# Performance work log

Measured on AMD Instinct MI355X. Metric: run time of the kernel, lower is better.

Reference implementation:

```python
import jax, jax.numpy as jnp
import numpy as np

B, S, D, H, L, DFF, NI, AD = 8, 512, 512, 8, 4, 2048, 20000, 128
DK = D // H


def _make_pe(max_len, d):
    pos = np.arange(max_len, dtype=np.float32)[:, None]
    div = np.exp(np.arange(0, d, 2, dtype=np.float32) * (-np.log(10000.0) / d))
    pe = np.zeros((max_len, d), dtype=np.float32)
    pe[:, 0::2] = np.sin(pos * div)
    pe[:, 1::2] = np.cos(pos * div)
    return jnp.asarray(pe)


def setup_inputs() -> dict:
    key = jax.random.key(0)
    ks = iter(jax.random.split(key, 64))
    def nrm(shape):
        return jax.random.normal(next(ks), shape, jnp.float32) * 0.02
    inp = {
        'item_ids': jax.random.randint(next(ks), (B, S), 0, NI),
        'audio_features': jax.random.normal(next(ks), (B, S, AD), jnp.float32),
        'is_organic': jax.random.bernoulli(next(ks), 0.5, (B, S)).astype(jnp.float32),
        'padding_mask': jnp.ones((B, 1, 1, S), jnp.float32),
        'emb_table': nrm((NI + 1, D)),
        'pe': _make_pe(S, D),
        'Wa1': nrm((AD, D)), 'ba1': jnp.zeros((D,)),
        'Wa2': nrm((D, D)), 'ba2': jnp.zeros((D,)),
        'Wf': nrm((2 * D, D)), 'bf': jnp.zeros((D,)),
        'Wq': nrm((L, D, D)), 'bq': jnp.zeros((L, D)),
        'Wk': nrm((L, D, D)), 'bk': jnp.zeros((L, D)),
        'Wv': nrm((L, D, D)), 'bv': jnp.zeros((L, D)),
        'Wo': nrm((L, D, D)), 'bo': jnp.zeros((L, D)),
        'worg': nrm((L, H)), 'borg': jnp.zeros((L, H)),
        'ln1s': jnp.ones((L, D)), 'ln1b': jnp.zeros((L, D)),
        'ln2s': jnp.ones((L, D)), 'ln2b': jnp.zeros((L, D)),
        'Wff1': nrm((L, D, DFF)), 'bff1': jnp.zeros((L, DFF)),
        'Wff2': nrm((L, DFF, D)), 'bff2': jnp.zeros((L, D)),
        'lnOs': jnp.ones((D,)), 'lnOb': jnp.zeros((D,)),
        'Wg': nrm((D + 1, D)), 'bg': jnp.zeros((D,)),
        'Wout': nrm((D, NI)), 'bout': jnp.zeros((NI,)),
    }
    return inp


def _ln(x, s, b, eps=1e-5):
    m = jnp.mean(x, -1, keepdims=True)
    v = jnp.mean((x - m) ** 2, -1, keepdims=True)
    return (x - m) * jax.lax.rsqrt(v + eps) * s + b


def reference(item_ids, audio_features, is_organic, padding_mask, emb_table, pe,
              Wa1, ba1, Wa2, ba2, Wf, bf, Wq, bq, Wk, bk, Wv, bv, Wo, bo,
              worg, borg, ln1s, ln1b, ln2s, ln2b, Wff1, bff1, Wff2, bff2,
              lnOs, lnOb, Wg, bg, Wout, bout):
    b_, s_ = item_ids.shape
    scale = 1.0 / np.sqrt(DK).astype(np.float32)
    tbl = emb_table.at[0].set(0.0)  # padding_idx=0
    item_emb = tbl[item_ids]                                    # (B,S,D)
    audio_emb = jax.nn.relu(audio_features @ Wa1 + ba1) @ Wa2 + ba2
    x = jax.nn.relu(jnp.concatenate([item_emb, audio_emb], -1) @ Wf + bf)
    x = x + pe[:s_]
    for l in range(L):
        q = (x @ Wq[l] + bq[l]).reshape(b_, s_, H, DK).transpose(0, 2, 1, 3)
        k = (x @ Wk[l] + bk[l]).reshape(b_, s_, H, DK).transpose(0, 2, 1, 3)
        v = (x @ Wv[l] + bv[l]).reshape(b_, s_, H, DK).transpose(0, 2, 1, 3)
        scores = jnp.einsum('bhqd,bhkd->bhqk', q, k) * scale    # (B,H,S,S)
        org = is_organic[:, :, None] * worg[l] + borg[l]        # (B,S,H)
        scores = scores + org.transpose(0, 2, 1)[..., None]     # per-query bias
        scores = jnp.where(padding_mask == 0, -1e9, scores)
        attn = jax.nn.softmax(scores, -1)
        ctx = jnp.einsum('bhqk,bhkd->bhqd', attn, v)
        ctx = ctx.transpose(0, 2, 1, 3).reshape(b_, s_, D)
        x = _ln(x + ctx @ Wo[l] + bo[l], ln1s[l], ln1b[l])
        ff = jax.nn.relu(x @ Wff1[l] + bff1[l]) @ Wff2[l] + bff2[l]
        x = _ln(x + ff, ln2s[l], ln2b[l])
    x = _ln(x, lnOs, lnOb)
    gate = jax.nn.sigmoid(jnp.concatenate([x, is_organic[..., None]], -1) @ Wg + bg)
    logits = (x * gate) @ Wout + bout                           # (B,S,NI)
    return logits
```

## Files before the change

kernel.cpp:

```cpp
#include <hip/hip_runtime.h>
#include <hip/hip_bf16.h>

typedef float f32x4 __attribute__((ext_vector_type(4)));
typedef __bf16 bf16x8 __attribute__((ext_vector_type(8)));

#define DEV __device__ __forceinline__

constexpr int B_ = 8, S_ = 512, D_ = 512, H_ = 8, L_ = 4, DFF_ = 2048, NI_ = 20000, AD_ = 128, DK_ = 64;
constexpr int N_ = B_ * S_;
constexpr int NOUT_PAD = 20096;

DEV void gload_lds16(const void* g, void* l) {
  __builtin_amdgcn_global_load_lds((const __attribute__((address_space(1))) unsigned int*)g,
                                   (__attribute__((address_space(3))) unsigned int*)l, 16, 0, 0);
}

DEV int xcd_swizzle(int bid, int nwg) {
  int q = nwg >> 3, r = nwg & 7;
  int x = bid & 7, idx = bid >> 3;
  int base = (x < r) ? x * (q + 1) : r * (q + 1) + (x - r) * q;
  return base + idx;
}

template<int BM, int BN, int OUT_BF16, int ACT, int NT>
__global__ __launch_bounds__(BM * 2)
void gemm_bt(const __hip_bfloat16* __restrict__ A, int lda, long aS1, long aS2,
             const __hip_bfloat16* __restrict__ Bm, int ldb, long bS1, long bS2,
             void* __restrict__ Cv, int ldc, long cS1, long cS2,
             const float* __restrict__ bias, long biasS2,
             int K, int Ncols, int bdiv)
{
  constexpr int BK = 32;
  constexpr int NW = BM / 32;
  constexpr int WTN = BN / 2, NJ = WTN / 16;
  __shared__ __align__(16) unsigned short smA[2][BM * BK];
  __shared__ __align__(16) unsigned short smB[2][BN * BK];

  const int z = blockIdx.z;
  const long za = (long)(z / bdiv) * aS1 + (long)(z % bdiv) * aS2;
  const long zb = (long)(z / bdiv) * bS1 + (long)(z % bdiv) * bS2;
  const long zc = (long)(z / bdiv) * cS1 + (long)(z % bdiv) * cS2;
  const __hip_bfloat16* Ab = A + za;
  const __hip_bfloat16* Bp = Bm + zb;
  const float* bp = bias ? bias + (long)(z % bdiv) * biasS2 : nullptr;

  const int nwg = gridDim.x * gridDim.y;
  const int bid = blockIdx.y * gridDim.x + blockIdx.x;
  const int wgid = xcd_swizzle(bid, nwg);
  const int m0 = (wgid % gridDim.x) * BM, n0 = (wgid / gridDim.x) * BN;

  const int tid = threadIdx.x, wv = tid >> 6, lane = tid & 63;
  const int l15 = lane & 15, l4 = lane >> 4;
  const int wm = (wv >> 1) * 64, wn = (wv & 1) * WTN;

  auto stage = [&](int buf, int k0) {
#pragma unroll
    for (int it = 0; it < BM / 16 / NW; ++it) {
      int c = (it * NW + wv) * 64 + lane;
      int row = c >> 2, cc = c & 3;
      gload_lds16((const void*)(Ab + (size_t)(m0 + row) * lda + k0 + cc * 8),
                  (void*)&smA[buf][(size_t)(it * NW + wv) * 512]);
    }
#pragma unroll
    for (int it = 0; it < BN / 16 / NW; ++it) {
      int c = (it * NW + wv) * 64 + lane;
      int row = c >> 2, cc = c & 3;
      gload_lds16((const void*)(Bp + (size_t)(n0 + row) * ldb + k0 + cc * 8),
                  (void*)&smB[buf][(size_t)(it * NW + wv) * 512]);
    }
  };

  f32x4 acc[4][NJ];
#pragma unroll
  for (int i = 0; i < 4; ++i)
#pragma unroll
    for (int j = 0; j < NJ; ++j) acc[i][j] = f32x4{0.f, 0.f, 0.f, 0.f};

  const int nk = K / BK;
  stage(0, 0);
  __syncthreads();

  int cur = 0;
  for (int t = 0; t < nk; ++t) {
    if (t + 1 < nk) stage(cur ^ 1, (t + 1) * BK);

    bf16x8 af[4], bfr[NJ];
#pragma unroll
    for (int i = 0; i < 4; ++i)
      af[i] = *reinterpret_cast<const bf16x8*>(&smA[cur][(wm + i * 16 + l15) * BK + l4 * 8]);
#pragma unroll
    for (int j = 0; j < NJ; ++j)
      bfr[j] = *reinterpret_cast<const bf16x8*>(&smB[cur][(wn + j * 16 + l15) * BK + l4 * 8]);
    __builtin_amdgcn_s_setprio(1);
#pragma unroll
    for (int i = 0; i < 4; ++i)
#pragma unroll
      for (int j = 0; j < NJ; ++j)
        acc[i][j] = __builtin_amdgcn_mfma_f32_16x16x32_bf16(af[i], bfr[j], acc[i][j], 0, 0, 0);
    __builtin_amdgcn_s_setprio(0);
    __syncthreads();
    cur ^= 1;
  }

#pragma unroll
  for (int i = 0; i < 4; ++i) {
#pragma unroll
    for (int j = 0; j < NJ; ++j) {
#pragma unroll
      for (int r = 0; r < 4; ++r) {
        int row = m0 + wm + i * 16 + l4 * 4 + r;
        int col = n0 + wn + j * 16 + l15;
        if (col < Ncols) {
          float v = acc[i][j][r];
          if (bp) v += bp[col];
          if (ACT == 1) v = v > 0.f ? v : 0.f;
          if constexpr (OUT_BF16) {
            ((__hip_bfloat16*)Cv)[zc + (size_t)row * ldc + col] = __float2bfloat16(v);
          } else {
            float* dst = &((float*)Cv)[zc + (size_t)row * ldc + col];
            if constexpr (NT) __builtin_nontemporal_store(v, dst);
            else *dst = v;
          }
        }
      }
    }
  }
}

__global__ __launch_bounds__(256)
void k_flash(const __hip_bfloat16* __restrict__ q, const __hip_bfloat16* __restrict__ k,
             const __hip_bfloat16* __restrict__ vt, const float* __restrict__ mask,
             __hip_bfloat16* __restrict__ ctx)
{
  __shared__ __align__(16) unsigned short Ql[64 * 64];
  __shared__ __align__(16) unsigned short Kl[2][64 * 64];
  __shared__ __align__(16) unsigned short Vl[2][64 * 64];
  __shared__ __align__(16) unsigned short Pl[4][16 * 64];

  const int qt = blockIdx.x, bh = blockIdx.y;
  const int b = bh >> 3, h = bh & 7;
  const int tid = threadIdx.x, wv = tid >> 6, lane = tid & 63;
  const int l15 = lane & 15, l4 = lane >> 4;
  const int q0 = qt * 64;

  const __hip_bfloat16* Qg = q + ((size_t)(b * 512 + q0) * 512) + h * 64;
  const __hip_bfloat16* Kg = k + ((size_t)(b * 512) * 512) + h * 64;
  const __hip_bfloat16* Vg = vt + ((size_t)bh * 64) * 512;
  const float* mk = mask + b * 512;

  auto stageQ = [&]() {
#pragma unroll
    for (int it = 0; it < 2; ++it) {
      int idx = it * 256 + wv * 64 + lane;
      int row = idx >> 3, c = idx & 7;
      gload_lds16((const void*)(Qg + (size_t)row * 512 + (c ^ (row & 7)) * 8),
                  (void*)&Ql[(it * 256 + wv * 64) * 8]);
    }
  };
  auto stageKV = [&](int buf, int kv0) {
#pragma unroll
    for (int it = 0; it < 2; ++it) {
      int idx = it * 256 + wv * 64 + lane;
      int row = idx >> 3, c = idx & 7;
      gload_lds16((const void*)(Kg + (size_t)(kv0 + row) * 512 + (c ^ (row & 7)) * 8),
                  (void*)&Kl[buf][(it * 256 + wv * 64) * 8]);
    }
#pragma unroll
    for (int it = 0; it < 2; ++it) {
      int idx = it * 256 + wv * 64 + lane;
      int row = idx >> 3, c = idx & 7;
      gload_lds16((const void*)(Vg + (size_t)row * 512 + kv0 + (c ^ (row & 7)) * 8),
                  (void*)&Vl[buf][(it * 256 + wv * 64) * 8]);
    }
  };

  stageQ();
  stageKV(0, 0);
  __syncthreads();

  bf16x8 aq[2];
#pragma unroll
  for (int kk = 0; kk < 2; ++kk) {
    int row = wv * 16 + l15;
    aq[kk] = *reinterpret_cast<const bf16x8*>(
        &Ql[row * 64 + (((kk * 4 + l4) ^ (row & 7)) * 8)]);
  }

  f32x4 accO[4];
  float mrun[4], lrun[4];
#pragma unroll
  for (int j = 0; j < 4; ++j) accO[j] = f32x4{0.f, 0.f, 0.f, 0.f};
#pragma unroll
  for (int r = 0; r < 4; ++r) { mrun[r] = -3e38f; lrun[r] = 0.f; }

  int cur = 0;
  for (int t = 0; t < 8; ++t) {
    if (t + 1 < 8) stageKV(cur ^ 1, (t + 1) * 64);
    const int kv0 = t * 64;

    f32x4 s[4];
#pragma unroll
    for (int j = 0; j < 4; ++j) s[j] = f32x4{0.f, 0.f, 0.f, 0.f};
#pragma unroll
    for (int kk = 0; kk < 2; ++kk) {
#pragma unroll
      for (int j = 0; j < 4; ++j) {
        int row = j * 16 + l15;
        bf16x8 bk = *reinterpret_cast<const bf16x8*>(
            &Kl[cur][row * 64 + (((kk * 4 + l4) ^ (row & 7)) * 8)]);
        s[j] = __builtin_amdgcn_mfma_f32_16x16x32_bf16(aq[kk], bk, s[j], 0, 0, 0);
      }
    }

#pragma unroll
    for (int j = 0; j < 4; ++j) {
      float mval = mk[kv0 + j * 16 + l15];
#pragma unroll
      for (int r = 0; r < 4; ++r)
        s[j][r] = (mval == 0.f) ? -1e30f : s[j][r];
    }

    float alpha[4];
#pragma unroll
    for (int r = 0; r < 4; ++r) {
      float v = fmaxf(fmaxf(s[0][r], s[1][r]), fmaxf(s[2][r], s[3][r]));
      v = fmaxf(v, __shfl_xor(v, 1));
      v = fmaxf(v, __shfl_xor(v, 2));
      v = fmaxf(v, __shfl_xor(v, 4));
      v = fmaxf(v, __shfl_xor(v, 8));
      float mn = fmaxf(mrun[r], v);
      alpha[r] = __expf(mrun[r] - mn);
      mrun[r] = mn;
    }
    float rs[4] = {0.f, 0.f, 0.f, 0.f};
#pragma unroll
    for (int j = 0; j < 4; ++j)
#pragma unroll
      for (int r = 0; r < 4; ++r) {
        float p = __expf(s[j][r] - mrun[r]);
        s[j][r] = p;
        rs[r] += p;
      }
#pragma unroll
    for (int r = 0; r < 4; ++r) {
      float v = rs[r];
      v += __shfl_xor(v, 1); v += __shfl_xor(v, 2);
      v += __shfl_xor(v, 4); v += __shfl_xor(v, 8);
      lrun[r] = lrun[r] * alpha[r] + v;
#pragma unroll
      for (int j = 0; j < 4; ++j) accO[j][r] *= alpha[r];
    }

#pragma unroll
    for (int j = 0; j < 4; ++j)
#pragma unroll
      for (int r = 0; r < 4; ++r) {
        int qrow = l4 * 4 + r, key = j * 16 + l15;
        __hip_bfloat16 hb = __float2bfloat16(s[j][r]);
        Pl[wv][qrow * 64 + (((key >> 3) ^ (qrow & 7)) * 8) + (key & 7)] =
            *reinterpret_cast<unsigned short*>(&hb);
      }

#pragma unroll
    for (int kc = 0; kc < 2; ++kc) {
      bf16x8 ap = *reinterpret_cast<const bf16x8*>(
          &Pl[wv][l15 * 64 + (((kc * 4 + l4) ^ (l15 & 7)) * 8)]);
#pragma unroll
      for (int j = 0; j < 4; ++j) {
        int row = j * 16 + l15;
        bf16x8 bv2 = *reinterpret_cast<const bf16x8*>(
            &Vl[cur][row * 64 + (((kc * 4 + l4) ^ (row & 7)) * 8)]);
        accO[j] = __builtin_amdgcn_mfma_f32_16x16x32_bf16(ap, bv2, accO[j], 0, 0, 0);
      }
    }
    __syncthreads();
    cur ^= 1;
  }

#pragma unroll
  for (int r = 0; r < 4; ++r) {
    float inv = lrun[r] > 0.f ? 1.f / lrun[r] : 0.f;
#pragma unroll
    for (int j = 0; j < 4; ++j) {
      int row = q0 + wv * 16 + l4 * 4 + r;
      int col = h * 64 + j * 16 + l15;
      ctx[(size_t)(b * 512 + row) * 512 + col] = __float2bfloat16(accO[j][r] * inv);
    }
  }
}

__global__ void k_transpose(const float* __restrict__ in, __hip_bfloat16* __restrict__ out,
                            int K, int N, long inBatch, long outBatch, float scale)
{
  __shared__ float tile[32][33];
  int z = blockIdx.z;
  const float* ip = in + (long)z * inBatch;
  __hip_bfloat16* op = out + (long)z * outBatch;
  int n0 = blockIdx.x * 32, k0 = blockIdx.y * 32;
  int tx = threadIdx.x, ty = threadIdx.y;
#pragma unroll
  for (int r = 0; r < 4; ++r) {
    int k = k0 + ty + r * 8, n = n0 + tx;
    if (k < K && n < N) tile[ty + r * 8][tx] = ip[(size_t)k * N + n];
  }
  __syncthreads();
#pragma unroll
  for (int r = 0; r < 4; ++r) {
    int n = n0 + ty + r * 8, k = k0 + tx;
    if (n < N && k < K) op[(size_t)n * K + k] = __float2bfloat16(tile[tx][ty + r * 8] * scale);
  }
}

__global__ void k_cvt(const float* __restrict__ in, __hip_bfloat16* __restrict__ out) {
  int i = blockIdx.x * 256 + threadIdx.x;
  out[i] = __float2bfloat16(in[i]);
}

__global__ void k_packbias(const float* __restrict__ bq, const float* __restrict__ bk,
                           const float* __restrict__ bv, float* __restrict__ out) {
  int i = blockIdx.x * 256 + threadIdx.x;
  int d = i & 511, t = (i >> 9) % 3, l = i / (3 * 512);
  const float* src = (t == 0) ? bq : (t == 1) ? bk : bv;
  out[i] = src[l * 512 + d] * (t == 0 ? 0.125f : 1.f);
}

__global__ void k_gather(const int* __restrict__ ids, const float* __restrict__ tbl,
                         __hip_bfloat16* __restrict__ cat) {
  int n = blockIdx.x, t = threadIdx.x;
  int id = ids[n];
  const float* src = tbl + (size_t)id * 512;
  size_t dst = (size_t)n * 1024;
  float a0 = (id == 0) ? 0.f : src[t];
  float a1 = (id == 0) ? 0.f : src[t + 256];
  cat[dst + t] = __float2bfloat16(a0);
  cat[dst + t + 256] = __float2bfloat16(a1);
}

__global__ void k_peadd(float* __restrict__ xf, __hip_bfloat16* __restrict__ xb,
                        const float* __restrict__ pe) {
  int i = blockIdx.x * 256 + threadIdx.x;
  float v = xf[i] + pe[i & (S_ * D_ - 1)];
  xf[i] = v;
  xb[i] = __float2bfloat16(v);
}

__global__ void k_vtrans(const __hip_bfloat16* __restrict__ v, __hip_bfloat16* __restrict__ vt) {
  int i = blockIdx.x * 256 + threadIdx.x;
  int s = i & 511, d = (i >> 9) & 63, h = (i >> 15) & 7, b = i >> 18;
  vt[i] = v[(size_t)((b << 9) + s) * 512 + (h << 6) + d];
}

__global__ void k_ln(const float* __restrict__ x, const float* __restrict__ y,
                     const float* __restrict__ gam, const float* __restrict__ bet,
                     float* __restrict__ xout, __hip_bfloat16* __restrict__ xb) {
  int row = blockIdx.x, t = threadIdx.x;
  size_t base = (size_t)row * 512;
  float v0 = x[base + t], v1 = x[base + t + 256];
  if (y) { v0 += y[base + t]; v1 += y[base + t + 256]; }
  __shared__ float sm[4];
  float s = v0 + v1;
  for (int o = 32; o; o >>= 1) s += __shfl_xor(s, o);
  if ((t & 63) == 0) sm[t >> 6] = s;
  __syncthreads();
  float mean = (sm[0] + sm[1] + sm[2] + sm[3]) * (1.f / 512.f);
  __syncthreads();
  float d0 = v0 - mean, d1 = v1 - mean;
  float qq = d0 * d0 + d1 * d1;
  for (int o = 32; o; o >>= 1) qq += __shfl_xor(qq, o);
  if ((t & 63) == 0) sm[t >> 6] = qq;
  __syncthreads();
  float var = (sm[0] + sm[1] + sm[2] + sm[3]) * (1.f / 512.f);
  float rs = rsqrtf(var + 1e-5f);
  float o0 = d0 * rs * gam[t] + bet[t];
  float o1 = d1 * rs * gam[t + 256] + bet[t + 256];
  xout[base + t] = o0;
  xout[base + t + 256] = o1;
  xb[base + t] = __float2bfloat16(o0);
  xb[base + t + 256] = __float2bfloat16(o1);
}

__global__ void k_gate(const float* __restrict__ xn, const float* __restrict__ g,
                       const float* __restrict__ org, const float* __restrict__ wgl,
                       __hip_bfloat16* __restrict__ xg) {
  int i = blockIdx.x * 256 + threadIdx.x;
  float zz = g[i] + org[i >> 9] * wgl[i & 511];
  float sg = 1.f / (1.f + expf(-zz));
  xg[i] = __float2bfloat16(xn[i] * sg);
}

extern "C" void kernel_launch(void* const* d_in, const int* in_sizes, int n_in,
                              void* d_out, int out_size, void* d_ws, size_t ws_size,
                              hipStream_t stream) {
  typedef __hip_bfloat16 bf;
  const int*   item_ids = (const int*)  d_in[0];
  const float* audio    = (const float*)d_in[1];
  const float* organic  = (const float*)d_in[2];
  const float* mask     = (const float*)d_in[3];
  const float* emb      = (const float*)d_in[4];
  const float* pe       = (const float*)d_in[5];
  const float* Wa1 = (const float*)d_in[6],  *ba1 = (const float*)d_in[7];
  const float* Wa2 = (const float*)d_in[8],  *ba2 = (const float*)d_in[9];
  const float* Wf  = (const float*)d_in[10], *bfb = (const float*)d_in[11];
  const float* Wq  = (const float*)d_in[12], *bq  = (const float*)d_in[13];
  const float* Wk  = (const float*)d_in[14], *bk  = (const float*)d_in[15];
  const float* Wv  = (const float*)d_in[16], *bv  = (const float*)d_in[17];
  const float* Wo  = (const float*)d_in[18], *bo  = (const float*)d_in[19];
  const float* ln1s = (const float*)d_in[22], *ln1b = (const float*)d_in[23];
  const float* ln2s = (const float*)d_in[24], *ln2b = (const float*)d_in[25];
  const float* Wff1 = (const float*)d_in[26], *bff1 = (const float*)d_in[27];
  const float* Wff2 = (const float*)d_in[28], *bff2 = (const float*)d_in[29];
  const float* lnOs = (const float*)d_in[30], *lnOb = (const float*)d_in[31];
  const float* Wg   = (const float*)d_in[32], *bg   = (const float*)d_in[33];
  const float* Wout = (const float*)d_in[34], *bout = (const float*)d_in[35];
  float* out = (float*)d_out;

  char* ws = (char*)d_ws;
  size_t off = 0;
  auto alloc = [&](size_t bytes) -> char* {
    char* p = ws + off;
    off = (off + bytes + 255) & ~(size_t)255;
    return p;
  };
  bf* Wa1T = (bf*)alloc((size_t)512 * 128 * 2);
  bf* Wa2T = (bf*)alloc((size_t)512 * 512 * 2);
  bf* WfT  = (bf*)alloc((size_t)512 * 1024 * 2);
  bf* WqkvT = (bf*)alloc((size_t)L_ * 3 * D_ * D_ * 2);
  bf* WoT  = (bf*)alloc((size_t)L_ * D_ * D_ * 2);
  bf* Wff1T = (bf*)alloc((size_t)L_ * DFF_ * D_ * 2);
  bf* Wff2T = (bf*)alloc((size_t)L_ * D_ * DFF_ * 2);
  bf* WgT   = (bf*)alloc((size_t)512 * 512 * 2);
  bf* WoutT = (bf*)alloc((size_t)NOUT_PAD * 512 * 2);
  float* bqkv = (float*)alloc((size_t)L_ * 3 * 512 * 4);
  bf* ab    = (bf*)alloc((size_t)N_ * AD_ * 2);
  bf* cat   = (bf*)alloc((size_t)N_ * 1024 * 2);
  bf* ah    = (bf*)alloc((size_t)N_ * 512 * 2);
  float* xf = (float*)alloc((size_t)N_ * 512 * 4);
  bf* xb    = (bf*)alloc((size_t)N_ * 512 * 2);
  bf* qkv   = (bf*)alloc((size_t)3 * N_ * 512 * 2);
  bf* vt    = (bf*)alloc((size_t)B_ * H_ * DK_ * S_ * 2);
  bf* ctxb  = (bf*)alloc((size_t)N_ * 512 * 2);
  float* ybuf = (float*)alloc((size_t)N_ * 512 * 4);
  bf* ff1b  = (bf*)alloc((size_t)N_ * DFF_ * 2);
  bf* xg    = (bf*)alloc((size_t)N_ * 512 * 2);
  if (off > ws_size) return;

  bf* qb = qkv;
  bf* kb = qkv + (size_t)N_ * 512;
  bf* vb = qkv + (size_t)2 * N_ * 512;

  dim3 tb(32, 8);
  k_transpose<<<dim3(16, 4, 1),  tb, 0, stream>>>(Wa1, Wa1T, 128, 512, 0, 0, 1.f);
  k_transpose<<<dim3(16, 16, 1), tb, 0, stream>>>(Wa2, Wa2T, 512, 512, 0, 0, 1.f);
  k_transpose<<<dim3(16, 32, 1), tb, 0, stream>>>(Wf, WfT, 1024, 512, 0, 0, 1.f);
  k_transpose<<<dim3(16, 16, L_), tb, 0, stream>>>(Wq, WqkvT, 512, 512,
      (long)D_ * D_, (long)3 * D_ * D_, 0.125f);
  k_transpose<<<dim3(16, 16, L_), tb, 0, stream>>>(Wk, WqkvT + (size_t)D_ * D_, 512, 512,
      (long)D_ * D_, (long)3 * D_ * D_, 1.f);
  k_transpose<<<dim3(16, 16, L_), tb, 0, stream>>>(Wv, WqkvT + (size_t)2 * D_ * D_, 512, 512,
      (long)D_ * D_, (long)3 * D_ * D_, 1.f);
  k_transpose<<<dim3(16, 16, L_), tb, 0, stream>>>(Wo, WoT, 512, 512, (long)D_ * D_, (long)D_ * D_, 1.f);
  k_transpose<<<dim3(64, 16, L_), tb, 0, stream>>>(Wff1, Wff1T, 512, 2048, (long)D_ * DFF_, (long)D_ * DFF_, 1.f);
  k_transpose<<<dim3(16, 64, L_), tb, 0, stream>>>(Wff2, Wff2T, 2048, 512, (long)DFF_ * D_, (long)DFF_ * D_, 1.f);
  k_transpose<<<dim3(16, 16, 1), tb, 0, stream>>>(Wg, WgT, 512, 512, 0, 0, 1.f);
  k_transpose<<<dim3(625, 16, 1), tb, 0, stream>>>(Wout, WoutT, 512, 20000, 0, 0, 1.f);
  k_packbias<<<(L_ * 3 * 512) / 256, 256, 0, stream>>>(bq, bk, bv, bqkv);

  k_cvt<<<(N_ * AD_) / 256, 256, 0, stream>>>(audio, ab);
  k_gather<<<N_, 256, 0, stream>>>(item_ids, emb, cat);
  gemm_bt<128, 64, 1, 1, 0><<<dim3(32, 8, 1), 256, 0, stream>>>(ab, 128, 0, 0, Wa1T, 128, 0, 0,
      (void*)ah, 512, 0, 0, ba1, 0, 128, 512, 1);
  gemm_bt<128, 64, 1, 0, 0><<<dim3(32, 8, 1), 256, 0, stream>>>(ah, 512, 0, 0, Wa2T, 512, 0, 0,
      (void*)(cat + 512), 1024, 0, 0, ba2, 0, 512, 512, 1);
  gemm_bt<128, 64, 0, 1, 0><<<dim3(32, 8, 1), 256, 0, stream>>>(cat, 1024, 0, 0, WfT, 1024, 0, 0,
      (void*)xf, 512, 0, 0, bfb, 0, 1024, 512, 1);
  k_peadd<<<(N_ * D_) / 256, 256, 0, stream>>>(xf, xb, pe);

  for (int l = 0; l < L_; ++l) {
    gemm_bt<128, 64, 1, 0, 0><<<dim3(32, 8, 3), 256, 0, stream>>>(xb, 512, 0, 0,
        WqkvT + (size_t)l * 3 * D_ * D_, 512, 0, (long)D_ * D_,
        (void*)qkv, 512, 0, (long)N_ * D_,
        bqkv + (size_t)l * 3 * 512, 512, 512, 512, 3);
    k_vtrans<<<(B_ * H_ * DK_ * S_) / 256, 256, 0, stream>>>(vb, vt);
    k_flash<<<dim3(8, B_ * H_), 256, 0, stream>>>(qb, kb, vt, mask, ctxb);
    gemm_bt<128, 64, 0, 0, 0><<<dim3(32, 8, 1), 256, 0, stream>>>(ctxb, 512, 0, 0,
        WoT + (size_t)l * D_ * D_, 512, 0, 0, (void*)ybuf, 512, 0, 0, bo + l * D_, 0, 512, 512, 1);
    k_ln<<<N_, 256, 0, stream>>>(xf, ybuf, ln1s + l * D_, ln1b + l * D_, xf, xb);
    gemm_bt<256, 128, 1, 1, 0><<<dim3(16, 16, 1), 512, 0, stream>>>(xb, 512, 0, 0,
        Wff1T + (size_t)l * DFF_ * D_, 512, 0, 0, (void*)ff1b, 2048, 0, 0, bff1 + l * DFF_, 0, 512, 2048, 1);
    gemm_bt<128, 64, 0, 0, 0><<<dim3(32, 8, 1), 256, 0, stream>>>(ff1b, 2048, 0, 0,
        Wff2T + (size_t)l * D_ * DFF_, 2048, 0, 0, (void*)ybuf, 512, 0, 0, bff2 + l * D_, 0, 2048, 512, 1);
    k_ln<<<N_, 256, 0, stream>>>(xf, ybuf, ln2s + l * D_, ln2b + l * D_, xf, xb);
  }

  k_ln<<<N_, 256, 0, stream>>>(xf, nullptr, lnOs, lnOb, xf, xb);
  gemm_bt<128, 64, 0, 0, 0><<<dim3(32, 8, 1), 256, 0, stream>>>(xb, 512, 0, 0, WgT, 512, 0, 0,
      (void*)ybuf, 512, 0, 0, bg, 0, 512, 512, 1);
  k_gate<<<(N_ * D_) / 256, 256, 0, stream>>>(xf, ybuf, organic, Wg + (size_t)512 * 512, xg);
  gemm_bt<256, 128, 0, 0, 1><<<dim3(16, 157, 1), 512, 0, stream>>>(xg, 512, 0, 0, WoutT, 512, 0, 0,
      (void*)out, 20000, 0, 0, bout, 0, 512, 20000, 1);
}
```

Baseline: 890.9 us.

## Replace double-buffered GEMM with 4-stage vmcnt-pipelined kernel and smaller tiles

The GEMM kernel moves from a double-buffered loop with two __syncthreads per k-step to a 4-buffer ring that keeps three k-tiles of global-to-LDS loads in flight. It waits with explicit s_waitcnt vmcnt counts and uses a single barrier per step. The FF1 and output-projection GEMMs also move from 256x128 tiles on 512 threads to 128x128 tiles on 256 threads, which doubles the grid. The aim is to hide global load latency and improve occupancy, at the cost of more LDS per block and hand-coded wait counts that must match the number of loads issued.

```diff
diff --git a/kernel.cpp b/kernel.cpp
--- a/kernel.cpp
+++ b/kernel.cpp
@@ -13,6 +13,14 @@
 DEV void gload_lds16(const void* g, void* l) {
   __builtin_amdgcn_global_load_lds((const __attribute__((address_space(1))) unsigned int*)g,
                                    (__attribute__((address_space(3))) unsigned int*)l, 16, 0, 0);
+}
+
+template<int N> DEV void waitv() {
+  if constexpr (N == 0)      asm volatile("s_waitcnt vmcnt(0)" ::: "memory");
+  else if constexpr (N == 3) asm volatile("s_waitcnt vmcnt(3)" ::: "memory");
+  else if constexpr (N == 4) asm volatile("s_waitcnt vmcnt(4)" ::: "memory");
+  else if constexpr (N == 6) asm volatile("s_waitcnt vmcnt(6)" ::: "memory");
+  else if constexpr (N == 8) asm volatile("s_waitcnt vmcnt(8)" ::: "memory");
 }
 
 DEV int xcd_swizzle(int bid, int nwg) {
@@ -23,18 +31,18 @@
 }
 
 template<int BM, int BN, int OUT_BF16, int ACT, int NT>
-__global__ __launch_bounds__(BM * 2)
-void gemm_bt(const __hip_bfloat16* __restrict__ A, int lda, long aS1, long aS2,
-             const __hip_bfloat16* __restrict__ Bm, int ldb, long bS1, long bS2,
-             void* __restrict__ Cv, int ldc, long cS1, long cS2,
-             const float* __restrict__ bias, long biasS2,
-             int K, int Ncols, int bdiv)
+__global__ __launch_bounds__(256)
+void gemm_p(const __hip_bfloat16* __restrict__ A, int lda, long aS1, long aS2,
+            const __hip_bfloat16* __restrict__ Bm, int ldb, long bS1, long bS2,
+            void* __restrict__ Cv, int ldc, long cS1, long cS2,
+            const float* __restrict__ bias, long biasS2,
+            int K, int Ncols, int bdiv)
 {
-  constexpr int BK = 32;
-  constexpr int NW = BM / 32;
-  constexpr int WTN = BN / 2, NJ = WTN / 16;
-  __shared__ __align__(16) unsigned short smA[2][BM * BK];
-  __shared__ __align__(16) unsigned short smB[2][BN * BK];
+  constexpr int BK = 32, NB = 4;
+  constexpr int MI = BM / 32, NJ = BN / 32;
+  constexpr int LT = BM / 64 + BN / 64;
+  __shared__ __align__(16) unsigned short smA[NB][BM * BK];
+  __shared__ __align__(16) unsigned short smB[NB][BN * BK];
 
   const int z = blockIdx.z;
   const long za = (long)(z / bdiv) * aS1 + (long)(z % bdiv) * aS2;
@@ -51,59 +59,64 @@
 
   const int tid = threadIdx.x, wv = tid >> 6, lane = tid & 63;
   const int l15 = lane & 15, l4 = lane >> 4;
-  const int wm = (wv >> 1) * 64, wn = (wv & 1) * WTN;
+  const int wm = (wv >> 1) * (BM / 2), wn = (wv & 1) * (BN / 2);
 
   auto stage = [&](int buf, int k0) {
 #pragma unroll
-    for (int it = 0; it < BM / 16 / NW; ++it) {
-      int c = (it * NW + wv) * 64 + lane;
+    for (int it = 0; it < BM / 64; ++it) {
+      int c = it * 256 + tid;
       int row = c >> 2, cc = c & 3;
       gload_lds16((const void*)(Ab + (size_t)(m0 + row) * lda + k0 + cc * 8),
-                  (void*)&smA[buf][(size_t)(it * NW + wv) * 512]);
-    }
-#pragma unroll
-    for (int it = 0; it < BN / 16 / NW; ++it) {
-      int c = (it * NW + wv) * 64 + lane;
+                  (void*)&smA[buf][(size_t)(it * 256 + wv * 64) * 8]);
+    }
+#pragma unroll
+    for (int it = 0; it < BN / 64; ++it) {
+      int c = it * 256 + tid;
       int row = c >> 2, cc = c & 3;
       gload_lds16((const void*)(Bp + (size_t)(n0 + row) * ldb + k0 + cc * 8),
-                  (void*)&smB[buf][(size_t)(it * NW + wv) * 512]);
+                  (void*)&smB[buf][(size_t)(it * 256 + wv * 64) * 8]);
     }
   };
 
-  f32x4 acc[4][NJ];
-#pragma unroll
-  for (int i = 0; i < 4; ++i)
+  f32x4 acc[MI][NJ];
+#pragma unroll
+  for (int i = 0; i < MI; ++i)
 #pragma unroll
     for (int j = 0; j < NJ; ++j) acc[i][j] = f32x4{0.f, 0.f, 0.f, 0.f};
 
   const int nk = K / BK;
   stage(0, 0);
-  __syncthreads();
-
-  int cur = 0;
+  stage(1, BK);
+  stage(2, 2 * BK);
+
   for (int t = 0; t < nk; ++t) {
-    if (t + 1 < nk) stage(cur ^ 1, (t + 1) * BK);
-
-    bf16x8 af[4], bfr[NJ];
-#pragma unroll
-    for (int i = 0; i < 4; ++i)
+    if (t + 2 < nk)      waitv<2 * LT>();
+    else if (t + 1 < nk) waitv<LT>();
+    else                 waitv<0>();
+    __builtin_amdgcn_s_barrier();
+    __builtin_amdgcn_sched_barrier(0);
+
+    if (t + 3 < nk) stage((t + 3) & 3, (t + 3) * BK);
+
+    const int cur = t & 3;
+    bf16x8 af[MI], bfr[NJ];
+#pragma unroll
+    for (int i = 0; i < MI; ++i)
       af[i] = *reinterpret_cast<const bf16x8*>(&smA[cur][(wm + i * 16 + l15) * BK + l4 * 8]);
 #pragma unroll
     for (int j = 0; j < NJ; ++j)
       bfr[j] = *reinterpret_cast<const bf16x8*>(&smB[cur][(wn + j * 16 + l15) * BK + l4 * 8]);
     __builtin_amdgcn_s_setprio(1);
 #pragma unroll
-    for (int i = 0; i < 4; ++i)
+    for (int i = 0; i < MI; ++i)
 #pragma unroll
       for (int j = 0; j < NJ; ++j)
         acc[i][j] = __builtin_amdgcn_mfma_f32_16x16x32_bf16(af[i], bfr[j], acc[i][j], 0, 0, 0);
     __builtin_amdgcn_s_setprio(0);
-    __syncthreads();
-    cur ^= 1;
-  }
-
-#pragma unroll
-  for (int i = 0; i < 4; ++i) {
+  }
+
+#pragma unroll
+  for (int i = 0; i < MI; ++i) {
 #pragma unroll
     for (int j = 0; j < NJ; ++j) {
 #pragma unroll
@@ -467,35 +480,35 @@
 
   k_cvt<<<(N_ * AD_) / 256, 256, 0, stream>>>(audio, ab);
   k_gather<<<N_, 256, 0, stream>>>(item_ids, emb, cat);
-  gemm_bt<128, 64, 1, 1, 0><<<dim3(32, 8, 1), 256, 0, stream>>>(ab, 128, 0, 0, Wa1T, 128, 0, 0,
+  gemm_p<128, 64, 1, 1, 0><<<dim3(32, 8, 1), 256, 0, stream>>>(ab, 128, 0, 0, Wa1T, 128, 0, 0,
       (void*)ah, 512, 0, 0, ba1, 0, 128, 512, 1);
-  gemm_bt<128, 64, 1, 0, 0><<<dim3(32, 8, 1), 256, 0, stream>>>(ah, 512, 0, 0, Wa2T, 512, 0, 0,
+  gemm_p<128, 64, 1, 0, 0><<<dim3(32, 8, 1), 256, 0, stream>>>(ah, 512, 0, 0, Wa2T, 512, 0, 0,
       (void*)(cat + 512), 1024, 0, 0, ba2, 0, 512, 512, 1);
-  gemm_bt<128, 64, 0, 1, 0><<<dim3(32, 8, 1), 256, 0, stream>>>(cat, 1024, 0, 0, WfT, 1024, 0, 0,
+  gemm_p<128, 64, 0, 1, 0><<<dim3(32, 8, 1), 256, 0, stream>>>(cat, 1024, 0, 0, WfT, 1024, 0, 0,
       (void*)xf, 512, 0, 0, bfb, 0, 1024, 512, 1);
   k_peadd<<<(N_ * D_) / 256, 256, 0, stream>>>(xf, xb, pe);
 
   for (int l = 0; l < L_; ++l) {
-    gemm_bt<128, 64, 1, 0, 0><<<dim3(32, 8, 3), 256, 0, stream>>>(xb, 512, 0, 0,
+    gemm_p<128, 64, 1, 0, 0><<<dim3(32, 8, 3), 256, 0, stream>>>(xb, 512, 0, 0,
         WqkvT + (size_t)l * 3 * D_ * D_, 512, 0, (long)D_ * D_,
         (void*)qkv, 512, 0, (long)N_ * D_,
         bqkv + (size_t)l * 3 * 512, 512, 512, 512, 3);
     k_vtrans<<<(B_ * H_ * DK_ * S_) / 256, 256, 0, stream>>>(vb, vt);
     k_flash<<<dim3(8, B_ * H_), 256, 0, stream>>>(qb, kb, vt, mask, ctxb);
-    gemm_bt<128, 64, 0, 0, 0><<<dim3(32, 8, 1), 256, 0, stream>>>(ctxb, 512, 0, 0,
+    gemm_p<128, 64, 0, 0, 0><<<dim3(32, 8, 1), 256, 0, stream>>>(ctxb, 512, 0, 0,
         WoT + (size_t)l * D_ * D_, 512, 0, 0, (void*)ybuf, 512, 0, 0, bo + l * D_, 0, 512, 512, 1);
     k_ln<<<N_, 256, 0, stream>>>(xf, ybuf, ln1s + l * D_, ln1b + l * D_, xf, xb);
-    gemm_bt<256, 128, 1, 1, 0><<<dim3(16, 16, 1), 512, 0, stream>>>(xb, 512, 0, 0,
+    gemm_p<128, 128, 1, 1, 0><<<dim3(32, 16, 1), 256, 0, stream>>>(xb, 512, 0, 0,
         Wff1T + (size_t)l * DFF_ * D_, 512, 0, 0, (void*)ff1b, 2048, 0, 0, bff1 + l * DFF_, 0, 512, 2048, 1);
-    gemm_bt<128, 64, 0, 0, 0><<<dim3(32, 8, 1), 256, 0, stream>>>(ff1b, 2048, 0, 0,
+    gemm_p<128, 64, 0, 0, 0><<<dim3(32, 8, 1), 256, 0, stream>>>(ff1b, 2048, 0, 0,
         Wff2T + (size_t)l * D_ * DFF_, 2048, 0, 0, (void*)ybuf, 512, 0, 0, bff2 + l * D_, 0, 2048, 512, 1);
     k_ln<<<N_, 256, 0, stream>>>(xf, ybuf, ln2s + l * D_, ln2b + l * D_, xf, xb);
   }
 
   k_ln<<<N_, 256, 0, stream>>>(xf, nullptr, lnOs, lnOb, xf, xb);
-  gemm_bt<128, 64, 0, 0, 0><<<dim3(32, 8, 1), 256, 0, stream>>>(xb, 512, 0, 0, WgT, 512, 0, 0,
+  gemm_p<128, 64, 0, 0, 0><<<dim3(32, 8, 1), 256, 0, stream>>>(xb, 512, 0, 0, WgT, 512, 0, 0,
       (void*)ybuf, 512, 0, 0, bg, 0, 512, 512, 1);
   k_gate<<<(N_ * D_) / 256, 256, 0, stream>>>(xf, ybuf, organic, Wg + (size_t)512 * 512, xg);
-  gemm_bt<256, 128, 0, 0, 1><<<dim3(16, 157, 1), 512, 0, stream>>>(xg, 512, 0, 0, WoutT, 512, 0, 0,
+  gemm_p<128, 128, 0, 0, 1><<<dim3(32, 157, 1), 256, 0, stream>>>(xg, 512, 0, 0, WoutT, 512, 0, 0,
       (void*)out, 20000, 0, 0, bout, 0, 512, 20000, 1);
 }
```

Measured after the change: 954.4 us. 1.07x slower.

## Add 256x256 eight-wave GEMM with split-K-half pipelining for FF1 and output projection

Applied to the files above, without the earlier changes.

Introduces a new GEMM kernel with 256x256 tiles, 8 waves, a double-buffered LDS split into two K-halves, and swizzled LDS layout. Global-to-LDS prefetch for the next tile is interleaved between four MFMA phases using explicit vmcnt waits, raw barriers and setprio. It replaces the 256x128 GEMM for the FF1 layer and the large vocab output projection, raising per-block reuse and reducing block count. The output weight padding grows to fit 256-column tiles. Risks include higher register pressure (128 accumulator floats per lane) and fragile hand-written wait counts.

```diff
diff --git a/kernel.cpp b/kernel.cpp
--- a/kernel.cpp
+++ b/kernel.cpp
@@ -8,18 +8,168 @@
 
 constexpr int B_ = 8, S_ = 512, D_ = 512, H_ = 8, L_ = 4, DFF_ = 2048, NI_ = 20000, AD_ = 128, DK_ = 64;
 constexpr int N_ = B_ * S_;
-constexpr int NOUT_PAD = 20096;
+constexpr int NOUT_PAD = 20224;
 
 DEV void gload_lds16(const void* g, void* l) {
   __builtin_amdgcn_global_load_lds((const __attribute__((address_space(1))) unsigned int*)g,
                                    (__attribute__((address_space(3))) unsigned int*)l, 16, 0, 0);
 }
+
+template<int N> DEV void waitv() {
+  if constexpr (N == 0)      asm volatile("s_waitcnt vmcnt(0)" ::: "memory");
+  else if constexpr (N == 2) asm volatile("s_waitcnt vmcnt(2)" ::: "memory");
+  else if constexpr (N == 4) asm volatile("s_waitcnt vmcnt(4)" ::: "memory");
+}
+DEV void barx() { asm volatile("s_barrier" ::: "memory"); }
 
 DEV int xcd_swizzle(int bid, int nwg) {
   int q = nwg >> 3, r = nwg & 7;
   int x = bid & 7, idx = bid >> 3;
   int base = (x < r) ? x * (q + 1) : r * (q + 1) + (x - r) * q;
   return base + idx;
+}
+
+template<int OUT_BF16, int ACT, int NT>
+__global__ __launch_bounds__(512)
+void gemm8(const __hip_bfloat16* __restrict__ A, int lda,
+           const __hip_bfloat16* __restrict__ Bm, int ldb,
+           void* __restrict__ Cv, int ldc,
+           const float* __restrict__ bias, int K, int Ncols)
+{
+  __shared__ __align__(16) unsigned short As[2][2][256 * 32];
+  __shared__ __align__(16) unsigned short Bs[2][2][256 * 32];
+
+  const int nwg = gridDim.x * gridDim.y;
+  const int bid = blockIdx.y * gridDim.x + blockIdx.x;
+  const int wgid = xcd_swizzle(bid, nwg);
+  const int m0 = (wgid % gridDim.x) * 256, n0 = (wgid / gridDim.x) * 256;
+
+  const int tid = threadIdx.x, wv = tid >> 6, lane = tid & 63;
+  const int l15 = lane & 15, l4 = lane >> 4;
+  const int wr = wv >> 2, wc = wv & 3;
+
+  auto stageA = [&](int buf, int kh, int kt) {
+#pragma unroll
+    for (int i2 = 0; i2 < 2; ++i2) {
+      int g = i2 * 512 + tid, rho = g >> 2, c = g & 3;
+      int sc = c ^ ((rho ^ (rho >> 2)) & 3);
+      gload_lds16((const void*)(A + (size_t)(m0 + rho) * lda + kt * 64 + kh * 32 + sc * 8),
+                  (void*)&As[buf][kh][(size_t)(i2 * 512 + wv * 64) * 8]);
+    }
+  };
+  auto stageB = [&](int buf, int kh, int kt) {
+#pragma unroll
+    for (int i2 = 0; i2 < 2; ++i2) {
+      int g = i2 * 512 + tid, rho = g >> 2, c = g & 3;
+      int sc = c ^ ((rho ^ (rho >> 2)) & 3);
+      gload_lds16((const void*)(Bm + (size_t)(n0 + rho) * ldb + kt * 64 + kh * 32 + sc * 8),
+                  (void*)&Bs[buf][kh][(size_t)(i2 * 512 + wv * 64) * 8]);
+    }
+  };
+  auto rdA = [&](int buf, int ks, int i) -> bf16x8 {
+    int row = wr * 128 + i * 16 + l15;
+    int c = l4 ^ ((row ^ (row >> 2)) & 3);
+    return *reinterpret_cast<const bf16x8*>(&As[buf][ks][row * 32 + c * 8]);
+  };
+  auto rdB = [&](int buf, int ks, int j) -> bf16x8 {
+    int row = wc * 64 + j * 16 + l15;
+    int c = l4 ^ ((row ^ (row >> 2)) & 3);
+    return *reinterpret_cast<const bf16x8*>(&Bs[buf][ks][row * 32 + c * 8]);
+  };
+
+  f32x4 acc[8][4];
+#pragma unroll
+  for (int i = 0; i < 8; ++i)
+#pragma unroll
+    for (int j = 0; j < 4; ++j) acc[i][j] = f32x4{0.f, 0.f, 0.f, 0.f};
+
+  const int nk = K / 64;
+  stageA(0, 0, 0); stageB(0, 0, 0); stageA(0, 1, 0); stageB(0, 1, 0);
+  __syncthreads();
+
+  for (int kt = 0; kt < nk; ++kt) {
+    const int buf = kt & 1, nb = buf ^ 1;
+    const bool pf = (kt + 1 < nk);
+    bf16x8 bh0[4], bh1[4], at[4];
+
+#pragma unroll
+    for (int i = 0; i < 4; ++i) at[i] = rdA(buf, 0, i);
+#pragma unroll
+    for (int j = 0; j < 4; ++j) bh0[j] = rdB(buf, 0, j);
+    if (pf) stageA(nb, 0, kt + 1);
+    __builtin_amdgcn_s_setprio(1);
+#pragma unroll
+    for (int i = 0; i < 4; ++i)
+#pragma unroll
+      for (int j = 0; j < 4; ++j)
+        acc[i][j] = __builtin_amdgcn_mfma_f32_16x16x32_bf16(at[i], bh0[j], acc[i][j], 0, 0, 0);
+    __builtin_amdgcn_s_setprio(0);
+    waitv<2>();
+    barx();
+
+#pragma unroll
+    for (int i = 0; i < 4; ++i) at[i] = rdA(buf, 1, i);
+#pragma unroll
+    for (int j = 0; j < 4; ++j) bh1[j] = rdB(buf, 1, j);
+    if (pf) stageB(nb, 0, kt + 1);
+    __builtin_amdgcn_s_setprio(1);
+#pragma unroll
+    for (int i = 0; i < 4; ++i)
+#pragma unroll
+      for (int j = 0; j < 4; ++j)
+        acc[i][j] = __builtin_amdgcn_mfma_f32_16x16x32_bf16(at[i], bh1[j], acc[i][j], 0, 0, 0);
+    __builtin_amdgcn_s_setprio(0);
+    barx();
+
+#pragma unroll
+    for (int i = 0; i < 4; ++i) at[i] = rdA(buf, 0, i + 4);
+    if (pf) stageA(nb, 1, kt + 1);
+    __builtin_amdgcn_s_setprio(1);
+#pragma unroll
+    for (int i = 0; i < 4; ++i)
+#pragma unroll
+      for (int j = 0; j < 4; ++j)
+        acc[i + 4][j] = __builtin_amdgcn_mfma_f32_16x16x32_bf16(at[i], bh0[j], acc[i + 4][j], 0, 0, 0);
+    __builtin_amdgcn_s_setprio(0);
+    barx();
+
+#pragma unroll
+    for (int i = 0; i < 4; ++i) at[i] = rdA(buf, 1, i + 4);
+    if (pf) stageB(nb, 1, kt + 1);
+    __builtin_amdgcn_s_setprio(1);
+#pragma unroll
+    for (int i = 0; i < 4; ++i)
+#pragma unroll
+      for (int j = 0; j < 4; ++j)
+        acc[i + 4][j] = __builtin_amdgcn_mfma_f32_16x16x32_bf16(at[i], bh1[j], acc[i + 4][j], 0, 0, 0);
+    __builtin_amdgcn_s_setprio(0);
+    waitv<4>();
+    barx();
+  }
+
+#pragma unroll
+  for (int i = 0; i < 8; ++i) {
+#pragma unroll
+    for (int j = 0; j < 4; ++j) {
+#pragma unroll
+      for (int r = 0; r < 4; ++r) {
+        int row = m0 + wr * 128 + i * 16 + l4 * 4 + r;
+        int col = n0 + wc * 64 + j * 16 + l15;
+        if (col < Ncols) {
+          float v = acc[i][j][r];
+          if (bias) v += bias[col];
+          if (ACT == 1) v = v > 0.f ? v : 0.f;
+          if constexpr (OUT_BF16) {
+            ((__hip_bfloat16*)Cv)[(size_t)row * ldc + col] = __float2bfloat16(v);
+          } else {
+            float* dst = &((float*)Cv)[(size_t)row * ldc + col];
+            if constexpr (NT) __builtin_nontemporal_store(v, dst);
+            else *dst = v;
+          }
+        }
+      }
+    }
+  }
 }
 
 template<int BM, int BN, int OUT_BF16, int ACT, int NT>
@@ -485,8 +635,8 @@
     gemm_bt<128, 64, 0, 0, 0><<<dim3(32, 8, 1), 256, 0, stream>>>(ctxb, 512, 0, 0,
         WoT + (size_t)l * D_ * D_, 512, 0, 0, (void*)ybuf, 512, 0, 0, bo + l * D_, 0, 512, 512, 1);
     k_ln<<<N_, 256, 0, stream>>>(xf, ybuf, ln1s + l * D_, ln1b + l * D_, xf, xb);
-    gemm_bt<256, 128, 1, 1, 0><<<dim3(16, 16, 1), 512, 0, stream>>>(xb, 512, 0, 0,
-        Wff1T + (size_t)l * DFF_ * D_, 512, 0, 0, (void*)ff1b, 2048, 0, 0, bff1 + l * DFF_, 0, 512, 2048, 1);
+    gemm8<1, 1, 0><<<dim3(16, 8), 512, 0, stream>>>(xb, 512,
+        Wff1T + (size_t)l * DFF_ * D_, 512, (void*)ff1b, 2048, bff1 + l * DFF_, 512, 2048);
     gemm_bt<128, 64, 0, 0, 0><<<dim3(32, 8, 1), 256, 0, stream>>>(ff1b, 2048, 0, 0,
         Wff2T + (size_t)l * D_ * DFF_, 2048, 0, 0, (void*)ybuf, 512, 0, 0, bff2 + l * D_, 0, 2048, 512, 1);
     k_ln<<<N_, 256, 0, stream>>>(xf, ybuf, ln2s + l * D_, ln2b + l * D_, xf, xb);
@@ -496,6 +646,6 @@
   gemm_bt<128, 64, 0, 0, 0><<<dim3(32, 8, 1), 256, 0, stream>>>(xb, 512, 0, 0, WgT, 512, 0, 0,
       (void*)ybuf, 512, 0, 0, bg, 0, 512, 512, 1);
   k_gate<<<(N_ * D_) / 256, 256, 0, stream>>>(xf, ybuf, organic, Wg + (size_t)512 * 512, xg);
-  gemm_bt<256, 128, 0, 0, 1><<<dim3(16, 157, 1), 512, 0, stream>>>(xg, 512, 0, 0, WoutT, 512, 0, 0,
-      (void*)out, 20000, 0, 0, bout, 0, 512, 20000, 1);
-}
+  gemm8<0, 0, 1><<<dim3(16, 79), 512, 0, stream>>>(xg, 512, WoutT, 512,
+      (void*)out, 20000, bout, 512, 20000);
+}
```

After: 926.2 us. 1.04x slower.

## Rewrite GEMM with BK=64 swizzled LDS and fuse epilogues for PE, V-transpose, gate

Applied to the files above, without the earlier changes.

Replaces the batched GEMM kernel with a new one that uses a K-tile of 64, an XOR-swizzled LDS layout to cut bank conflicts, and 256-thread blocks for all tile shapes. Positional-encoding add, V transpose and sigmoid gating move into GEMM epilogues, which removes three elementwise kernels and their global round trips. QKV now runs as one wide GEMM with a scatter epilogue. The FFN1 and output GEMMs change from 256x128 to 128x128 tiles, trading per-block reuse for more blocks, and the transposed V store is strided, which may hurt coalescing.

```diff
diff --git a/kernel.cpp b/kernel.cpp
--- a/kernel.cpp
+++ b/kernel.cpp
@@ -22,27 +22,21 @@
   return base + idx;
 }
 
-template<int BM, int BN, int OUT_BF16, int ACT, int NT>
-__global__ __launch_bounds__(BM * 2)
-void gemm_bt(const __hip_bfloat16* __restrict__ A, int lda, long aS1, long aS2,
-             const __hip_bfloat16* __restrict__ Bm, int ldb, long bS1, long bS2,
-             void* __restrict__ Cv, int ldc, long cS1, long cS2,
-             const float* __restrict__ bias, long biasS2,
-             int K, int Ncols, int bdiv)
+template<int BM, int BN, int EPI, int ACT, int NT>
+__global__ __launch_bounds__(256)
+void gemm2(const __hip_bfloat16* __restrict__ A, int lda,
+           const __hip_bfloat16* __restrict__ Bm, int ldb,
+           void* __restrict__ Cv, int ldc,
+           const float* __restrict__ bias,
+           const void* __restrict__ p1, const void* __restrict__ p2,
+           const void* __restrict__ p3,
+           int K, int Ncols)
 {
-  constexpr int BK = 32;
-  constexpr int NW = BM / 32;
-  constexpr int WTN = BN / 2, NJ = WTN / 16;
+  constexpr int BK = 64;
+  constexpr int MI = BM / 32, NJ = BN / 32;
+  constexpr int LA = BM * BK / 2048, LB = BN * BK / 2048;
   __shared__ __align__(16) unsigned short smA[2][BM * BK];
   __shared__ __align__(16) unsigned short smB[2][BN * BK];
-
-  const int z = blockIdx.z;
-  const long za = (long)(z / bdiv) * aS1 + (long)(z % bdiv) * aS2;
-  const long zb = (long)(z / bdiv) * bS1 + (long)(z % bdiv) * bS2;
-  const long zc = (long)(z / bdiv) * cS1 + (long)(z % bdiv) * cS2;
-  const __hip_bfloat16* Ab = A + za;
-  const __hip_bfloat16* Bp = Bm + zb;
-  const float* bp = bias ? bias + (long)(z % bdiv) * biasS2 : nullptr;
 
   const int nwg = gridDim.x * gridDim.y;
   const int bid = blockIdx.y * gridDim.x + blockIdx.x;
@@ -51,28 +45,28 @@
 
   const int tid = threadIdx.x, wv = tid >> 6, lane = tid & 63;
   const int l15 = lane & 15, l4 = lane >> 4;
-  const int wm = (wv >> 1) * 64, wn = (wv & 1) * WTN;
+  const int wm = (wv >> 1) * (BM / 2), wn = (wv & 1) * (BN / 2);
 
   auto stage = [&](int buf, int k0) {
 #pragma unroll
-    for (int it = 0; it < BM / 16 / NW; ++it) {
-      int c = (it * NW + wv) * 64 + lane;
-      int row = c >> 2, cc = c & 3;
-      gload_lds16((const void*)(Ab + (size_t)(m0 + row) * lda + k0 + cc * 8),
-                  (void*)&smA[buf][(size_t)(it * NW + wv) * 512]);
-    }
-#pragma unroll
-    for (int it = 0; it < BN / 16 / NW; ++it) {
-      int c = (it * NW + wv) * 64 + lane;
-      int row = c >> 2, cc = c & 3;
-      gload_lds16((const void*)(Bp + (size_t)(n0 + row) * ldb + k0 + cc * 8),
-                  (void*)&smB[buf][(size_t)(it * NW + wv) * 512]);
+    for (int it = 0; it < LA; ++it) {
+      int idx = it * 256 + tid, row = idx >> 3, c = idx & 7;
+      int sc = c ^ (row & 7);
+      gload_lds16((const void*)(A + (size_t)(m0 + row) * lda + k0 + sc * 8),
+                  (void*)&smA[buf][(size_t)(it * 256 + wv * 64) * 8]);
+    }
+#pragma unroll
+    for (int it = 0; it < LB; ++it) {
+      int idx = it * 256 + tid, row = idx >> 3, c = idx & 7;
+      int sc = c ^ (row & 7);
+      gload_lds16((const void*)(Bm + (size_t)(n0 + row) * ldb + k0 + sc * 8),
+                  (void*)&smB[buf][(size_t)(it * 256 + wv * 64) * 8]);
     }
   };
 
-  f32x4 acc[4][NJ];
-#pragma unroll
-  for (int i = 0; i < 4; ++i)
+  f32x4 acc[MI][NJ];
+#pragma unroll
+  for (int i = 0; i < MI; ++i)
 #pragma unroll
     for (int j = 0; j < NJ; ++j) acc[i][j] = f32x4{0.f, 0.f, 0.f, 0.f};
 
@@ -84,26 +78,38 @@
   for (int t = 0; t < nk; ++t) {
     if (t + 1 < nk) stage(cur ^ 1, (t + 1) * BK);
 
-    bf16x8 af[4], bfr[NJ];
-#pragma unroll
-    for (int i = 0; i < 4; ++i)
-      af[i] = *reinterpret_cast<const bf16x8*>(&smA[cur][(wm + i * 16 + l15) * BK + l4 * 8]);
+    bf16x8 af[MI][2], bfr[NJ][2];
+#pragma unroll
+    for (int i = 0; i < MI; ++i)
+#pragma unroll
+      for (int kk = 0; kk < 2; ++kk) {
+        int row = wm + i * 16 + l15;
+        int ch = (kk * 4 + l4) ^ (row & 7);
+        af[i][kk] = *reinterpret_cast<const bf16x8*>(&smA[cur][row * BK + ch * 8]);
+      }
 #pragma unroll
     for (int j = 0; j < NJ; ++j)
-      bfr[j] = *reinterpret_cast<const bf16x8*>(&smB[cur][(wn + j * 16 + l15) * BK + l4 * 8]);
+#pragma unroll
+      for (int kk = 0; kk < 2; ++kk) {
+        int row = wn + j * 16 + l15;
+        int ch = (kk * 4 + l4) ^ (row & 7);
+        bfr[j][kk] = *reinterpret_cast<const bf16x8*>(&smB[cur][row * BK + ch * 8]);
+      }
     __builtin_amdgcn_s_setprio(1);
 #pragma unroll
-    for (int i = 0; i < 4; ++i)
-#pragma unroll
-      for (int j = 0; j < NJ; ++j)
-        acc[i][j] = __builtin_amdgcn_mfma_f32_16x16x32_bf16(af[i], bfr[j], acc[i][j], 0, 0, 0);
+    for (int kk = 0; kk < 2; ++kk)
+#pragma unroll
+      for (int i = 0; i < MI; ++i)
+#pragma unroll
+        for (int j = 0; j < NJ; ++j)
+          acc[i][j] = __builtin_amdgcn_mfma_f32_16x16x32_bf16(af[i][kk], bfr[j][kk], acc[i][j], 0, 0, 0);
     __builtin_amdgcn_s_setprio(0);
     __syncthreads();
     cur ^= 1;
   }
 
 #pragma unroll
-  for (int i = 0; i < 4; ++i) {
+  for (int i = 0; i < MI; ++i) {
 #pragma unroll
     for (int j = 0; j < NJ; ++j) {
 #pragma unroll
@@ -112,14 +118,32 @@
         int col = n0 + wn + j * 16 + l15;
         if (col < Ncols) {
           float v = acc[i][j][r];
-          if (bp) v += bp[col];
+          if (bias) v += bias[col];
           if (ACT == 1) v = v > 0.f ? v : 0.f;
-          if constexpr (OUT_BF16) {
-            ((__hip_bfloat16*)Cv)[zc + (size_t)row * ldc + col] = __float2bfloat16(v);
-          } else {
-            float* dst = &((float*)Cv)[zc + (size_t)row * ldc + col];
+          if constexpr (EPI == 0) {
+            float* dst = &((float*)Cv)[(size_t)row * ldc + col];
             if constexpr (NT) __builtin_nontemporal_store(v, dst);
             else *dst = v;
+          } else if constexpr (EPI == 1) {
+            ((__hip_bfloat16*)Cv)[(size_t)row * ldc + col] = __float2bfloat16(v);
+          } else if constexpr (EPI == 2) {
+            v += ((const float*)p2)[(size_t)(row & 511) * 512 + col];
+            ((float*)Cv)[(size_t)row * ldc + col] = v;
+            ((__hip_bfloat16*)p1)[(size_t)row * ldc + col] = __float2bfloat16(v);
+          } else if constexpr (EPI == 3) {
+            if (col < 1024) {
+              ((__hip_bfloat16*)Cv)[(size_t)(col >> 9) * N_ * 512 + (size_t)row * 512 + (col & 511)] =
+                  __float2bfloat16(v);
+            } else {
+              int hd = col - 1024, b = row >> 9, s = row & 511;
+              ((__hip_bfloat16*)p1)[((size_t)(b * 8 + (hd >> 6)) * 64 + (hd & 63)) * 512 + s] =
+                  __float2bfloat16(v);
+            }
+          } else if constexpr (EPI == 4) {
+            float zz = v + ((const float*)p2)[row] * ((const float*)p3)[col];
+            float sg = 1.f / (1.f + __expf(-zz));
+            float xn = ((const float*)p1)[(size_t)row * 512 + col];
+            ((__hip_bfloat16*)Cv)[(size_t)row * 512 + col] = __float2bfloat16(xn * sg);
           }
         }
       }
@@ -334,20 +358,6 @@
   float a1 = (id == 0) ? 0.f : src[t + 256];
   cat[dst + t] = __float2bfloat16(a0);
   cat[dst + t + 256] = __float2bfloat16(a1);
-}
-
-__global__ void k_peadd(float* __restrict__ xf, __hip_bfloat16* __restrict__ xb,
-                        const float* __restrict__ pe) {
-  int i = blockIdx.x * 256 + threadIdx.x;
-  float v = xf[i] + pe[i & (S_ * D_ - 1)];
-  xf[i] = v;
-  xb[i] = __float2bfloat16(v);
-}
-
-__global__ void k_vtrans(const __hip_bfloat16* __restrict__ v, __hip_bfloat16* __restrict__ vt) {
-  int i = blockIdx.x * 256 + threadIdx.x;
-  int s = i & 511, d = (i >> 9) & 63, h = (i >> 15) & 7, b = i >> 18;
-  vt[i] = v[(size_t)((b << 9) + s) * 512 + (h << 6) + d];
 }
 
 __global__ void k_ln(const float* __restrict__ x, const float* __restrict__ y,
@@ -377,15 +387,6 @@
   xout[base + t + 256] = o1;
   xb[base + t] = __float2bfloat16(o0);
   xb[base + t + 256] = __float2bfloat16(o1);
-}
-
-__global__ void k_gate(const float* __restrict__ xn, const float* __restrict__ g,
-                       const float* __restrict__ org, const float* __restrict__ wgl,
-                       __hip_bfloat16* __restrict__ xg) {
-  int i = blockIdx.x * 256 + threadIdx.x;
-  float zz = g[i] + org[i >> 9] * wgl[i & 511];
-  float sg = 1.f / (1.f + expf(-zz));
-  xg[i] = __float2bfloat16(xn[i] * sg);
 }
 
 extern "C" void kernel_launch(void* const* d_in, const int* in_sizes, int n_in,
@@ -446,7 +447,6 @@
 
   bf* qb = qkv;
   bf* kb = qkv + (size_t)N_ * 512;
-  bf* vb = qkv + (size_t)2 * N_ * 512;
 
   dim3 tb(32, 8);
   k_transpose<<<dim3(16, 4, 1),  tb, 0, stream>>>(Wa1, Wa1T, 128, 512, 0, 0, 1.f);
@@ -467,35 +467,35 @@
 
   k_cvt<<<(N_ * AD_) / 256, 256, 0, stream>>>(audio, ab);
   k_gather<<<N_, 256, 0, stream>>>(item_ids, emb, cat);
-  gemm_bt<128, 64, 1, 1, 0><<<dim3(32, 8, 1), 256, 0, stream>>>(ab, 128, 0, 0, Wa1T, 128, 0, 0,
-      (void*)ah, 512, 0, 0, ba1, 0, 128, 512, 1);
-  gemm_bt<128, 64, 1, 0, 0><<<dim3(32, 8, 1), 256, 0, stream>>>(ah, 512, 0, 0, Wa2T, 512, 0, 0,
-      (void*)(cat + 512), 1024, 0, 0, ba2, 0, 512, 512, 1);
-  gemm_bt<128, 64, 0, 1, 0><<<dim3(32, 8, 1), 256, 0, stream>>>(cat, 1024, 0, 0, WfT, 1024, 0, 0,
-      (void*)xf, 512, 0, 0, bfb, 0, 1024, 512, 1);
-  k_peadd<<<(N_ * D_) / 256, 256, 0, stream>>>(xf, xb, pe);
+  gemm2<128, 64, 1, 1, 0><<<dim3(32, 8), 256, 0, stream>>>(ab, 128, Wa1T, 128,
+      (void*)ah, 512, ba1, nullptr, nullptr, nullptr, 128, 512);
+  gemm2<128, 64, 1, 0, 0><<<dim3(32, 8), 256, 0, stream>>>(ah, 512, Wa2T, 512,
+      (void*)(cat + 512), 1024, ba2, nullptr, nullptr, nullptr, 512, 512);
+  gemm2<128, 64, 2, 1, 0><<<dim3(32, 8), 256, 0, stream>>>(cat, 1024, WfT, 1024,
+      (void*)xf, 512, bfb, (void*)xb, (const void*)pe, nullptr, 1024, 512);
 
   for (int l = 0; l < L_; ++l) {
-    gemm_bt<128, 64, 1, 0, 0><<<dim3(32, 8, 3), 256, 0, stream>>>(xb, 512, 0, 0,
-        WqkvT + (size_t)l * 3 * D_ * D_, 512, 0, (long)D_ * D_,
-        (void*)qkv, 512, 0, (long)N_ * D_,
-        bqkv + (size_t)l * 3 * 512, 512, 512, 512, 3);
-    k_vtrans<<<(B_ * H_ * DK_ * S_) / 256, 256, 0, stream>>>(vb, vt);
+    gemm2<128, 64, 3, 0, 0><<<dim3(32, 24), 256, 0, stream>>>(xb, 512,
+        WqkvT + (size_t)l * 3 * D_ * D_, 512, (void*)qkv, 512,
+        bqkv + (size_t)l * 3 * 512, (void*)vt, nullptr, nullptr, 512, 1536);
     k_flash<<<dim3(8, B_ * H_), 256, 0, stream>>>(qb, kb, vt, mask, ctxb);
-    gemm_bt<128, 64, 0, 0, 0><<<dim3(32, 8, 1), 256, 0, stream>>>(ctxb, 512, 0, 0,
-        WoT + (size_t)l * D_ * D_, 512, 0, 0, (void*)ybuf, 512, 0, 0, bo + l * D_, 0, 512, 512, 1);
+    gemm2<128, 64, 0, 0, 0><<<dim3(32, 8), 256, 0, stream>>>(ctxb, 512,
+        WoT + (size_t)l * D_ * D_, 512, (void*)ybuf, 512, bo + l * D_,
+        nullptr, nullptr, nullptr, 512, 512);
     k_ln<<<N_, 256, 0, stream>>>(xf, ybuf, ln1s + l * D_, ln1b + l * D_, xf, xb);
-    gemm_bt<256, 128, 1, 1, 0><<<dim3(16, 16, 1), 512, 0, stream>>>(xb, 512, 0, 0,
-        Wff1T + (size_t)l * DFF_ * D_, 512, 0, 0, (void*)ff1b, 2048, 0, 0, bff1 + l * DFF_, 0, 512, 2048, 1);
-    gemm_bt<128, 64, 0, 0, 0><<<dim3(32, 8, 1), 256, 0, stream>>>(ff1b, 2048, 0, 0,
-        Wff2T + (size_t)l * D_ * DFF_, 2048, 0, 0, (void*)ybuf, 512, 0, 0, bff2 + l * D_, 0, 2048, 512, 1);
+    gemm2<128, 128, 1, 1, 0><<<dim3(32, 16), 256, 0, stream>>>(xb, 512,
+        Wff1T + (size_t)l * DFF_ * D_, 512, (void*)ff1b, 2048, bff1 + l * DFF_,
+        nullptr, nullptr, nullptr, 512, 2048);
+    gemm2<128, 64, 0, 0, 0><<<dim3(32, 8), 256, 0, stream>>>(ff1b, 2048,
+        Wff2T + (size_t)l * D_ * DFF_, 2048, (void*)ybuf, 512, bff2 + l * D_,
+        nullptr, nullptr, nullptr, 2048, 512);
     k_ln<<<N_, 256, 0, stream>>>(xf, ybuf, ln2s + l * D_, ln2b + l * D_, xf, xb);
   }
 
   k_ln<<<N_, 256, 0, stream>>>(xf, nullptr, lnOs, lnOb, xf, xb);
-  gemm_bt<128, 64, 0, 0, 0><<<dim3(32, 8, 1), 256, 0, stream>>>(xb, 512, 0, 0, WgT, 512, 0, 0,
-      (void*)ybuf, 512, 0, 0, bg, 0, 512, 512, 1);
-  k_gate<<<(N_ * D_) / 256, 256, 0, stream>>>(xf, ybuf, organic, Wg + (size_t)512 * 512, xg);
-  gemm_bt<256, 128, 0, 0, 1><<<dim3(16, 157, 1), 512, 0, stream>>>(xg, 512, 0, 0, WoutT, 512, 0, 0,
-      (void*)out, 20000, 0, 0, bout, 0, 512, 20000, 1);
-}
+  gemm2<128, 64, 4, 0, 0><<<dim3(32, 8), 256, 0, stream>>>(xb, 512, WgT, 512,
+      (void*)xg, 512, bg, (const void*)xf, (const void*)organic,
+      (const void*)(Wg + (size_t)512 * 512), 512, 512);
+  gemm2<128, 128, 0, 0, 1><<<dim3(32, 157), 256, 0, stream>>>(xg, 512, WoutT, 512,
+      (void*)out, 20000, bout, nullptr, nullptr, nullptr, 512, 20000);
+}
```

Result: faster. 861.1 us (-3.3%).
